# Kernel tuning notes

Measured on AMD Instinct MI355X. Metric: run time of the kernel, lower is better.

The kernel has to match this reference:

```python
import jax, jax.numpy as jnp
import numpy as np

D_MODEL = 1024
NUM_HEADS = 16
HEAD_DIM = D_MODEL // NUM_HEADS


def setup_inputs() -> dict:
    key = jax.random.key(0)
    ks = jax.random.split(key, 9)
    s = 1.0 / np.sqrt(D_MODEL)
    x = jax.random.normal(ks[0], (2, 2048, D_MODEL), dtype=jnp.float32)
    Wq = jax.random.normal(ks[1], (D_MODEL, D_MODEL), dtype=jnp.float32) * s
    Wk = jax.random.normal(ks[2], (D_MODEL, D_MODEL), dtype=jnp.float32) * s
    Wv = jax.random.normal(ks[3], (D_MODEL, D_MODEL), dtype=jnp.float32) * s
    Wo = jax.random.normal(ks[4], (D_MODEL, D_MODEL), dtype=jnp.float32) * s
    bq = jax.random.normal(ks[5], (D_MODEL,), dtype=jnp.float32) * s
    bk = jax.random.normal(ks[6], (D_MODEL,), dtype=jnp.float32) * s
    bv = jax.random.normal(ks[7], (D_MODEL,), dtype=jnp.float32) * s
    bo = jax.random.normal(ks[8], (D_MODEL,), dtype=jnp.float32) * s
    return {"x": x, "Wq": Wq, "bq": bq, "Wk": Wk, "bk": bk, "Wv": Wv, "bv": bv, "Wo": Wo, "bo": bo}


def reference(x, Wq, bq, Wk, bk, Wv, bv, Wo, bo):
    B, S, D = x.shape
    H, Hd = NUM_HEADS, HEAD_DIM
    # QKV projections
    q = (x @ Wq + bq).reshape(B, S, H, Hd).transpose(0, 2, 1, 3)  # [B,H,S,Hd]
    k = (x @ Wk + bk).reshape(B, S, H, Hd).transpose(0, 2, 1, 3)
    v = (x @ Wv + bv).reshape(B, S, H, Hd).transpose(0, 2, 1, 3)
    scores = jnp.einsum("bhqd,bhkd->bhqk", q, k) / jnp.sqrt(jnp.float32(Hd))
    attn = jax.nn.softmax(scores, axis=-1)
    out = jnp.einsum("bhqk,bhkd->bhqd", attn, v)  # [B,H,S,Hd]
    out = out.transpose(0, 2, 1, 3).reshape(B, S, D)
    return out @ Wo + bo
```

## Files before the change

kernel.cpp:

```cpp
#include <hip/hip_runtime.h>
#include <hip/hip_bf16.h>


typedef unsigned short u16;

#define D_MODEL 1024
#define NHEAD 16
#define HDIM 64
#define BATCH 2
#define SEQ 2048
#define MTOT (BATCH * SEQ)

#define QSCALE 0.18033688011112042f

using frag_ab = __attribute__((ext_vector_type(8))) short;
using frag_s4 = __attribute__((ext_vector_type(4))) short;
using frag_cd = __attribute__((ext_vector_type(4))) float;

__device__ __forceinline__ u16 f2u(float f) {
    union { float f; unsigned int i; } x;
    x.f = f;
    unsigned int r = x.i + 0x7fffu + ((x.i >> 16) & 1u);
    return (u16)(r >> 16);
}
__device__ __forceinline__ unsigned int pkrn(float a, float b) {
    union { __hip_bfloat162 h; unsigned int u; } c;
    c.h = __float22bfloat162_rn(float2{a, b});
    return c.u;
}

__global__ void prep(const float* __restrict__ W0, const float* __restrict__ W1,
                     const float* __restrict__ W2, const float* __restrict__ W3,
                     const float* __restrict__ X, u16* __restrict__ Wt,
                     u16* __restrict__ Xb) {
    const int z = blockIdx.z;
    const int tx = threadIdx.x, ty = threadIdx.y;
    if (z < 4) {
        __shared__ u16 t[32][33];
        const float* W = (z == 0) ? W0 : (z == 1) ? W1 : (z == 2) ? W2 : W3;
        u16* o = Wt + (size_t)z * D_MODEL * D_MODEL;
        int n0 = blockIdx.x * 32, k0 = blockIdx.y * 32;
        #pragma unroll
        for (int i = ty; i < 32; i += 8) t[i][tx] = f2u(W[(size_t)(k0 + i) * D_MODEL + n0 + tx]);
        __syncthreads();
        #pragma unroll
        for (int i = ty; i < 32; i += 8) o[(size_t)(n0 + i) * D_MODEL + k0 + tx] = t[tx][i];
    } else {
        int tid = ty * 32 + tx;
        size_t base = ((size_t)(blockIdx.y * 32 + blockIdx.x) * 256 + tid) * 16;
        #pragma unroll
        for (int c = 0; c < 4; ++c) {
            float4 v = *(const float4*)&X[base + c * 4];
            ushort4 o;
            o.x = f2u(v.x); o.y = f2u(v.y); o.z = f2u(v.z); o.w = f2u(v.w);
            *(ushort4*)&Xb[base + c * 4] = o;
        }
    }
}

__launch_bounds__(256, 3)
__global__ void gemm_qkvt(const u16* __restrict__ xb, const u16* __restrict__ Wt,
                          const float* __restrict__ bq, const float* __restrict__ bk,
                          const float* __restrict__ bv, u16* __restrict__ QKw,
                          u16* __restrict__ Vtw) {
    constexpr int BK = 64;
    __shared__ __attribute__((aligned(16))) u16 As[128 * BK];
    __shared__ __attribute__((aligned(16))) u16 Bs[128 * BK];

    const int tid = threadIdx.x;
    const int w = tid >> 6;
    const int lane = tid & 63;
    const int lrow = lane & 15, lquad = lane >> 4;
    const size_t WSZ = (size_t)D_MODEL * D_MODEL;

    const int bid = blockIdx.x;
    const bool vt = bid >= 512;
    const int z = vt ? 2 : (bid >> 8);
    const int t = vt ? (bid - 512) : (bid & 255);
    const int n0 = vt ? (t & 31) * 128 : (t & 7) * 128;
    const int m0 = vt ? (t >> 5) * 128 : (t >> 3) * 128;
    const u16* Ap = vt ? (Wt + 2 * WSZ) : xb;
    const u16* Bp = vt ? xb : (Wt + (size_t)z * WSZ);
    const float* bias = vt ? bv : (z ? bk : bq);

    frag_cd acc[4][4];
    #pragma unroll
    for (int i = 0; i < 4; i++)
        #pragma unroll
        for (int j = 0; j < 4; j++) acc[i][j] = (frag_cd){0.f, 0.f, 0.f, 0.f};

    const int wm = (w >> 1) * 64, wn = (w & 1) * 64;

    for (int k0 = 0; k0 < D_MODEL; k0 += BK) {
        __syncthreads();
        #pragma unroll
        for (int it = 0; it < 4; ++it) {
            int c = it * 256 + tid;
            int r = c >> 3, c8 = c & 7;
            const u16* ga = Ap + (size_t)(m0 + r) * D_MODEL + k0 + c8 * 8;
            char* la = (char*)As + (it * 256 + w * 64) * 16;
            __builtin_amdgcn_global_load_lds((const __attribute__((address_space(1))) void*)ga,
                                             (__attribute__((address_space(3))) void*)la, 16, 0, 0);
            const u16* gb = Bp + (size_t)(n0 + r) * D_MODEL + k0 + c8 * 8;
            char* lb = (char*)Bs + (it * 256 + w * 64) * 16;
            __builtin_amdgcn_global_load_lds((const __attribute__((address_space(1))) void*)gb,
                                             (__attribute__((address_space(3))) void*)lb, 16, 0, 0);
        }
        __syncthreads();

        #pragma unroll
        for (int kc = 0; kc < 2; ++kc) {
            frag_ab av[4], bvv[4];
            #pragma unroll
            for (int i = 0; i < 4; i++)
                av[i] = *(const frag_ab*)&As[(wm + i * 16 + lrow) * BK + kc * 32 + lquad * 8];
            #pragma unroll
            for (int j = 0; j < 4; j++)
                bvv[j] = *(const frag_ab*)&Bs[(wn + j * 16 + lrow) * BK + kc * 32 + lquad * 8];
            #pragma unroll
            for (int i = 0; i < 4; i++)
                #pragma unroll
                for (int j = 0; j < 4; j++)
                    acc[i][j] = __builtin_amdgcn_mfma_f32_16x16x32_bf16(av[i], bvv[j], acc[i][j], 0, 0, 0);
        }
    }

    const float scale = (!vt && z == 0) ? QSCALE : 1.0f;
    #pragma unroll
    for (int j = 0; j < 4; j++) {
        int gn = n0 + wn + j * 16 + lrow;
        #pragma unroll
        for (int i = 0; i < 4; i++) {
            #pragma unroll
            for (int rr = 0; rr < 4; ++rr) {
                int gm = m0 + wm + i * 16 + lquad * 4 + rr;
                if (!vt) {
                    float v = (acc[i][j][rr] + bias[gn]) * scale;
                    u16* oz = QKw + (size_t)z * ((size_t)MTOT * D_MODEL);
                    int b = gm >> 11, s = gm & (SEQ - 1);
                    int h = gn >> 6, d = gn & (HDIM - 1);
                    oz[(((size_t)(b * NHEAD + h)) * SEQ + s) * HDIM + d] = f2u(v);
                } else {
                    float v = acc[i][j][rr] + bias[gm];
                    int h = gm >> 6, d = gm & (HDIM - 1);
                    int b = gn >> 11, s = gn & (SEQ - 1);
                    Vtw[(((size_t)(b * NHEAD + h)) * HDIM + d) * SEQ + s] = f2u(v);
                }
            }
        }
    }
}

__launch_bounds__(256, 2)
__global__ void gemm_out(const u16* __restrict__ A, const u16* __restrict__ Wt,
                         const float* __restrict__ bias, float* __restrict__ out) {
    constexpr int BK = 64;
    __shared__ __attribute__((aligned(16))) u16 As[64 * BK];
    __shared__ __attribute__((aligned(16))) u16 Bs[128 * BK];

    const int tid = threadIdx.x;
    const int w = tid >> 6;
    const int lane = tid & 63;
    const int lrow = lane & 15, lquad = lane >> 4;
    const int m0 = blockIdx.y * 64, n0 = blockIdx.x * 128;

    frag_cd acc[2][4];
    #pragma unroll
    for (int i = 0; i < 2; i++)
        #pragma unroll
        for (int j = 0; j < 4; j++) acc[i][j] = (frag_cd){0.f, 0.f, 0.f, 0.f};

    const int wm = (w >> 1) * 32, wn = (w & 1) * 64;

    for (int k0 = 0; k0 < D_MODEL; k0 += BK) {
        __syncthreads();
        #pragma unroll
        for (int it = 0; it < 2; ++it) {
            int c = it * 256 + tid;
            int r = c >> 3, c8 = c & 7;
            const u16* ga = A + (size_t)(m0 + r) * D_MODEL + k0 + c8 * 8;
            char* la = (char*)As + (it * 256 + w * 64) * 16;
            __builtin_amdgcn_global_load_lds((const __attribute__((address_space(1))) void*)ga,
                                             (__attribute__((address_space(3))) void*)la, 16, 0, 0);
        }
        #pragma unroll
        for (int it = 0; it < 4; ++it) {
            int c = it * 256 + tid;
            int r = c >> 3, c8 = c & 7;
            const u16* gb = Wt + (size_t)(n0 + r) * D_MODEL + k0 + c8 * 8;
            char* lb = (char*)Bs + (it * 256 + w * 64) * 16;
            __builtin_amdgcn_global_load_lds((const __attribute__((address_space(1))) void*)gb,
                                             (__attribute__((address_space(3))) void*)lb, 16, 0, 0);
        }
        __syncthreads();

        #pragma unroll
        for (int kc = 0; kc < 2; ++kc) {
            frag_ab av[2], bvv[4];
            #pragma unroll
            for (int i = 0; i < 2; i++)
                av[i] = *(const frag_ab*)&As[(wm + i * 16 + lrow) * BK + kc * 32 + lquad * 8];
            #pragma unroll
            for (int j = 0; j < 4; j++)
                bvv[j] = *(const frag_ab*)&Bs[(wn + j * 16 + lrow) * BK + kc * 32 + lquad * 8];
            #pragma unroll
            for (int i = 0; i < 2; i++)
                #pragma unroll
                for (int j = 0; j < 4; j++)
                    acc[i][j] = __builtin_amdgcn_mfma_f32_16x16x32_bf16(av[i], bvv[j], acc[i][j], 0, 0, 0);
        }
    }

    #pragma unroll
    for (int j = 0; j < 4; j++) {
        int gn = n0 + wn + j * 16 + lrow;
        float bvf = bias[gn];
        #pragma unroll
        for (int i = 0; i < 2; i++)
            #pragma unroll
            for (int rr = 0; rr < 4; ++rr) {
                int gm = m0 + wm + i * 16 + lquad * 4 + rr;
                out[(size_t)gm * D_MODEL + gn] = acc[i][j][rr] + bvf;
            }
    }
}

__launch_bounds__(512, 4)
__global__ void attn_kernel(const u16* __restrict__ Q, const u16* __restrict__ K,
                            const u16* __restrict__ Vt, u16* __restrict__ O) {
    __shared__ __attribute__((aligned(16))) u16 Ks[2][128 * 64];
    __shared__ __attribute__((aligned(16))) u16 Vs[2][64 * 128];

    const int tid = threadIdx.x;
    const int w = tid >> 6;
    const int lane = tid & 63;
    const int lrow = lane & 15, lquad = lane >> 4;
    const int bh = blockIdx.y;
    const int q0 = blockIdx.x * 128;
    const size_t base = (size_t)bh * SEQ * HDIM;
    const u16* Qg = Q + base;
    const u16* Kg = K + base;
    const u16* Vg = Vt + base;

    frag_ab qf[2];
    #pragma unroll
    for (int kc = 0; kc < 2; ++kc)
        qf[kc] = *(const frag_ab*)&Qg[(size_t)(q0 + w * 16 + lrow) * HDIM + kc * 32 + lquad * 8];

    frag_cd accOT[4];
    #pragma unroll
    for (int df = 0; df < 4; df++) accOT[df] = (frag_cd){0.f, 0.f, 0.f, 0.f};
    float lacc = 0.f;

    auto stage = [&](int bsel, int kt2) {
        const u16* Kt = Kg + (size_t)(kt2 * 128) * HDIM;
        #pragma unroll
        for (int it = 0; it < 2; ++it) {
            const int c = it * 512 + tid;
            const int rk = c >> 3, ck = c & 7;
            const u16* gk = Kt + rk * HDIM + ((ck ^ (rk & 7)) << 3);
            char* lk = (char*)&Ks[bsel][0] + (it * 512 + w * 64) * 16;
            __builtin_amdgcn_global_load_lds((const __attribute__((address_space(1))) void*)gk,
                                             (__attribute__((address_space(3))) void*)lk, 16, 0, 0);
            const int rv = c >> 4, gv = c & 15;
            const u16* gvp = Vg + (size_t)rv * SEQ + kt2 * 128 + ((gv ^ (rv & 7)) << 3);
            char* lv = (char*)&Vs[bsel][0] + (it * 512 + w * 64) * 16;
            __builtin_amdgcn_global_load_lds((const __attribute__((address_space(1))) void*)gvp,
                                             (__attribute__((address_space(3))) void*)lv, 16, 0, 0);
        }
    };

    stage(0, 0);
    __syncthreads();

    int buf = 0;
    for (int kt = 0; kt < SEQ / 128; ++kt) {
        if (kt + 1 < SEQ / 128) stage(buf ^ 1, kt + 1);

        const u16* Ksb = &Ks[buf][0];
        const u16* Vsb = &Vs[buf][0];

        frag_cd sc[8];
        #pragma unroll
        for (int mf = 0; mf < 8; mf++) sc[mf] = (frag_cd){0.f, 0.f, 0.f, 0.f};
        #pragma unroll
        for (int kc = 0; kc < 2; ++kc) {
            const int cswz = (((kc << 2) + lquad) ^ (lrow & 7)) << 3;
            #pragma unroll
            for (int mf = 0; mf < 8; mf++) {
                frag_ab kf = *(const frag_ab*)&Ksb[(mf * 16 + lrow) * 64 + cswz];
                sc[mf] = __builtin_amdgcn_mfma_f32_16x16x32_bf16(kf, qf[kc], sc[mf], 0, 0, 0);
            }
        }

        frag_s4 pk[8];
        #pragma unroll
        for (int mf = 0; mf < 8; mf++) {
            float e0 = exp2f(sc[mf][0]), e1 = exp2f(sc[mf][1]);
            float e2 = exp2f(sc[mf][2]), e3 = exp2f(sc[mf][3]);
            lacc += (e0 + e1) + (e2 + e3);
            union { frag_s4 s; unsigned int u[2]; } pu;
            pu.u[0] = pkrn(e0, e1);
            pu.u[1] = pkrn(e2, e3);
            pk[mf] = pu.s;
        }

        #pragma unroll
        for (int mf = 0; mf < 8; mf++) {
            const int g = 2 * mf + (lquad >> 1);
            #pragma unroll
            for (int df = 0; df < 4; df++) {
                const int dr = df * 16 + lrow;
                frag_s4 vf = *(const frag_s4*)&Vsb[dr * 128 + ((g ^ (lrow & 7)) << 3) + (lquad & 1) * 4];
                accOT[df] = __builtin_amdgcn_mfma_f32_16x16x16bf16_1k(vf, pk[mf], accOT[df], 0, 0, 0);
            }
        }

        __syncthreads();
        buf ^= 1;
    }

    lacc += __shfl_xor(lacc, 16);
    lacc += __shfl_xor(lacc, 32);

    const int b = bh >> 4, h = bh & (NHEAD - 1);
    const int s = q0 + w * 16 + lrow;
    const float inv = 1.0f / lacc;
    u16* orow = O + ((size_t)(b * SEQ + s)) * D_MODEL + h * HDIM;
    #pragma unroll
    for (int df = 0; df < 4; df++) {
        union { unsigned int u[2]; ushort4 s4; } o;
        o.u[0] = pkrn(accOT[df][0] * inv, accOT[df][1] * inv);
        o.u[1] = pkrn(accOT[df][2] * inv, accOT[df][3] * inv);
        *(ushort4*)&orow[df * 16 + lquad * 4] = o.s4;
    }
}

extern "C" void kernel_launch(void* const* d_in, const int* in_sizes, int n_in,
                              void* d_out, int out_size, void* d_ws, size_t ws_size,
                              hipStream_t stream) {
    const float* x  = (const float*)d_in[0];
    const float* Wq = (const float*)d_in[1];
    const float* bq = (const float*)d_in[2];
    const float* Wk = (const float*)d_in[3];
    const float* bk = (const float*)d_in[4];
    const float* Wv = (const float*)d_in[5];
    const float* bv = (const float*)d_in[6];
    const float* Wo = (const float*)d_in[7];
    const float* bo = (const float*)d_in[8];

    u16* ws = (u16*)d_ws;
    const size_t WSZ = (size_t)D_MODEL * D_MODEL;
    const size_t TSZ = (size_t)MTOT * D_MODEL;
    u16* xb  = ws;
    u16* Wt  = ws + 4 * WSZ;
    u16* QKw = ws + 8 * WSZ;
    u16* Vtw = QKw + 2 * TSZ;
    u16* Aw  = Vtw + TSZ;

    prep<<<dim3(32, 32, 5), dim3(32, 8), 0, stream>>>(Wq, Wk, Wv, Wo, x, Wt, xb);
    gemm_qkvt<<<dim3(768), 256, 0, stream>>>(xb, Wt, bq, bk, bv, QKw, Vtw);
    attn_kernel<<<dim3(16, 32), 512, 0, stream>>>(QKw, QKw + TSZ, Vtw, Aw);
    gemm_out<<<dim3(8, 64), 256, 0, stream>>>(Aw, Wt + 3 * WSZ, bo, (float*)d_out);
}
```

Baseline: 218.6 us.

## Give each attention wave two query tiles to reuse K/V fragments

Halves the attention block to 4 waves, with each wave handling two 16-row query groups, so every K and V fragment read from LDS feeds two MFMAs instead of one. The staging loop now runs 4 iterations per thread to fill the same 128-key tile. This is meant to cut LDS read traffic per MFMA and raise arithmetic intensity. In exchange it roughly doubles accumulator and score registers per wave and halves wave-level parallelism per block, which may lower occupancy and latency hiding.

```diff
diff --git a/kernel.cpp b/kernel.cpp
--- a/kernel.cpp
+++ b/kernel.cpp
@@ -225,7 +225,7 @@
     }
 }
 
-__launch_bounds__(512, 4)
+__launch_bounds__(256, 2)
 __global__ void attn_kernel(const u16* __restrict__ Q, const u16* __restrict__ K,
                             const u16* __restrict__ Vt, u16* __restrict__ O) {
     __shared__ __attribute__((aligned(16))) u16 Ks[2][128 * 64];
@@ -242,29 +242,33 @@
     const u16* Kg = K + base;
     const u16* Vg = Vt + base;
 
-    frag_ab qf[2];
-    #pragma unroll
-    for (int kc = 0; kc < 2; ++kc)
-        qf[kc] = *(const frag_ab*)&Qg[(size_t)(q0 + w * 16 + lrow) * HDIM + kc * 32 + lquad * 8];
-
-    frag_cd accOT[4];
-    #pragma unroll
-    for (int df = 0; df < 4; df++) accOT[df] = (frag_cd){0.f, 0.f, 0.f, 0.f};
-    float lacc = 0.f;
+    frag_ab qf[2][2];
+    #pragma unroll
+    for (int g = 0; g < 2; ++g)
+        #pragma unroll
+        for (int kc = 0; kc < 2; ++kc)
+            qf[g][kc] = *(const frag_ab*)&Qg[(size_t)(q0 + g * 64 + w * 16 + lrow) * HDIM + kc * 32 + lquad * 8];
+
+    frag_cd accOT[2][4];
+    #pragma unroll
+    for (int g = 0; g < 2; ++g)
+        #pragma unroll
+        for (int df = 0; df < 4; df++) accOT[g][df] = (frag_cd){0.f, 0.f, 0.f, 0.f};
+    float lacc[2] = {0.f, 0.f};
 
     auto stage = [&](int bsel, int kt2) {
         const u16* Kt = Kg + (size_t)(kt2 * 128) * HDIM;
         #pragma unroll
-        for (int it = 0; it < 2; ++it) {
-            const int c = it * 512 + tid;
+        for (int it = 0; it < 4; ++it) {
+            const int c = it * 256 + tid;
             const int rk = c >> 3, ck = c & 7;
             const u16* gk = Kt + rk * HDIM + ((ck ^ (rk & 7)) << 3);
-            char* lk = (char*)&Ks[bsel][0] + (it * 512 + w * 64) * 16;
+            char* lk = (char*)&Ks[bsel][0] + (it * 256 + w * 64) * 16;
             __builtin_amdgcn_global_load_lds((const __attribute__((address_space(1))) void*)gk,
                                              (__attribute__((address_space(3))) void*)lk, 16, 0, 0);
             const int rv = c >> 4, gv = c & 15;
             const u16* gvp = Vg + (size_t)rv * SEQ + kt2 * 128 + ((gv ^ (rv & 7)) << 3);
-            char* lv = (char*)&Vs[bsel][0] + (it * 512 + w * 64) * 16;
+            char* lv = (char*)&Vs[bsel][0] + (it * 256 + w * 64) * 16;
             __builtin_amdgcn_global_load_lds((const __attribute__((address_space(1))) void*)gvp,
                                              (__attribute__((address_space(3))) void*)lv, 16, 0, 0);
         }
@@ -280,39 +284,45 @@
         const u16* Ksb = &Ks[buf][0];
         const u16* Vsb = &Vs[buf][0];
 
-        frag_cd sc[8];
-        #pragma unroll
-        for (int mf = 0; mf < 8; mf++) sc[mf] = (frag_cd){0.f, 0.f, 0.f, 0.f};
+        frag_cd sc[2][8];
+        #pragma unroll
+        for (int g = 0; g < 2; ++g)
+            #pragma unroll
+            for (int mf = 0; mf < 8; mf++) sc[g][mf] = (frag_cd){0.f, 0.f, 0.f, 0.f};
         #pragma unroll
         for (int kc = 0; kc < 2; ++kc) {
             const int cswz = (((kc << 2) + lquad) ^ (lrow & 7)) << 3;
             #pragma unroll
             for (int mf = 0; mf < 8; mf++) {
                 frag_ab kf = *(const frag_ab*)&Ksb[(mf * 16 + lrow) * 64 + cswz];
-                sc[mf] = __builtin_amdgcn_mfma_f32_16x16x32_bf16(kf, qf[kc], sc[mf], 0, 0, 0);
-            }
-        }
-
-        frag_s4 pk[8];
+                sc[0][mf] = __builtin_amdgcn_mfma_f32_16x16x32_bf16(kf, qf[0][kc], sc[0][mf], 0, 0, 0);
+                sc[1][mf] = __builtin_amdgcn_mfma_f32_16x16x32_bf16(kf, qf[1][kc], sc[1][mf], 0, 0, 0);
+            }
+        }
+
+        frag_s4 pk[2][8];
+        #pragma unroll
+        for (int g = 0; g < 2; ++g)
+            #pragma unroll
+            for (int mf = 0; mf < 8; mf++) {
+                float e0 = exp2f(sc[g][mf][0]), e1 = exp2f(sc[g][mf][1]);
+                float e2 = exp2f(sc[g][mf][2]), e3 = exp2f(sc[g][mf][3]);
+                lacc[g] += (e0 + e1) + (e2 + e3);
+                union { frag_s4 s; unsigned int u[2]; } pu;
+                pu.u[0] = pkrn(e0, e1);
+                pu.u[1] = pkrn(e2, e3);
+                pk[g][mf] = pu.s;
+            }
+
         #pragma unroll
         for (int mf = 0; mf < 8; mf++) {
-            float e0 = exp2f(sc[mf][0]), e1 = exp2f(sc[mf][1]);
-            float e2 = exp2f(sc[mf][2]), e3 = exp2f(sc[mf][3]);
-            lacc += (e0 + e1) + (e2 + e3);
-            union { frag_s4 s; unsigned int u[2]; } pu;
-            pu.u[0] = pkrn(e0, e1);
-            pu.u[1] = pkrn(e2, e3);
-            pk[mf] = pu.s;
-        }
-
-        #pragma unroll
-        for (int mf = 0; mf < 8; mf++) {
-            const int g = 2 * mf + (lquad >> 1);
+            const int gc = 2 * mf + (lquad >> 1);
             #pragma unroll
             for (int df = 0; df < 4; df++) {
                 const int dr = df * 16 + lrow;
-                frag_s4 vf = *(const frag_s4*)&Vsb[dr * 128 + ((g ^ (lrow & 7)) << 3) + (lquad & 1) * 4];
-                accOT[df] = __builtin_amdgcn_mfma_f32_16x16x16bf16_1k(vf, pk[mf], accOT[df], 0, 0, 0);
+                frag_s4 vf = *(const frag_s4*)&Vsb[dr * 128 + ((gc ^ (lrow & 7)) << 3) + (lquad & 1) * 4];
+                accOT[0][df] = __builtin_amdgcn_mfma_f32_16x16x16bf16_1k(vf, pk[0][mf], accOT[0][df], 0, 0, 0);
+                accOT[1][df] = __builtin_amdgcn_mfma_f32_16x16x16bf16_1k(vf, pk[1][mf], accOT[1][df], 0, 0, 0);
             }
         }
 
@@ -320,19 +330,25 @@
         buf ^= 1;
     }
 
-    lacc += __shfl_xor(lacc, 16);
-    lacc += __shfl_xor(lacc, 32);
+    #pragma unroll
+    for (int g = 0; g < 2; ++g) {
+        lacc[g] += __shfl_xor(lacc[g], 16);
+        lacc[g] += __shfl_xor(lacc[g], 32);
+    }
 
     const int b = bh >> 4, h = bh & (NHEAD - 1);
-    const int s = q0 + w * 16 + lrow;
-    const float inv = 1.0f / lacc;
-    u16* orow = O + ((size_t)(b * SEQ + s)) * D_MODEL + h * HDIM;
-    #pragma unroll
-    for (int df = 0; df < 4; df++) {
-        union { unsigned int u[2]; ushort4 s4; } o;
-        o.u[0] = pkrn(accOT[df][0] * inv, accOT[df][1] * inv);
-        o.u[1] = pkrn(accOT[df][2] * inv, accOT[df][3] * inv);
-        *(ushort4*)&orow[df * 16 + lquad * 4] = o.s4;
+    #pragma unroll
+    for (int g = 0; g < 2; ++g) {
+        const int s = q0 + g * 64 + w * 16 + lrow;
+        const float inv = 1.0f / lacc[g];
+        u16* orow = O + ((size_t)(b * SEQ + s)) * D_MODEL + h * HDIM;
+        #pragma unroll
+        for (int df = 0; df < 4; df++) {
+            union { unsigned int u[2]; ushort4 s4; } o;
+            o.u[0] = pkrn(accOT[g][df][0] * inv, accOT[g][df][1] * inv);
+            o.u[1] = pkrn(accOT[g][df][2] * inv, accOT[g][df][3] * inv);
+            *(ushort4*)&orow[df * 16 + lquad * 4] = o.s4;
+        }
     }
 }
 
@@ -360,6 +376,6 @@
 
     prep<<<dim3(32, 32, 5), dim3(32, 8), 0, stream>>>(Wq, Wk, Wv, Wo, x, Wt, xb);
     gemm_qkvt<<<dim3(768), 256, 0, stream>>>(xb, Wt, bq, bk, bv, QKw, Vtw);
-    attn_kernel<<<dim3(16, 32), 512, 0, stream>>>(QKw, QKw + TSZ, Vtw, Aw);
+    attn_kernel<<<dim3(16, 32), 256, 0, stream>>>(QKw, QKw + TSZ, Vtw, Aw);
     gemm_out<<<dim3(8, 64), 256, 0, stream>>>(Aw, Wt + 3 * WSZ, bo, (float*)d_out);
 }
```

Result: slower. 232.4 us (+6.3%).

## Split attention key range across warp halves with single-buffered LDS and combine

Applied to the files above, without the earlier changes.

The attention kernel now gives each block 64 queries instead of 128. Its eight warps form four query groups, and the two halves of the warps each handle half of every 128-key tile. Partial outputs and row sums are combined through LDS at the end. The LDS double buffer is dropped for a single buffer with two barriers per tile, which halves shared memory so that launch bounds can allow 8 blocks. The grid doubles to give more blocks and more occupancy. In exchange, K/V global traffic per query doubles and load latency is no longer overlapped with compute through prefetch.

```diff
diff --git a/kernel.cpp b/kernel.cpp
--- a/kernel.cpp
+++ b/kernel.cpp
@@ -16,6 +16,7 @@
 using frag_ab = __attribute__((ext_vector_type(8))) short;
 using frag_s4 = __attribute__((ext_vector_type(4))) short;
 using frag_cd = __attribute__((ext_vector_type(4))) float;
+using f32x2   = __attribute__((ext_vector_type(2))) float;
 
 __device__ __forceinline__ u16 f2u(float f) {
     union { float f; unsigned int i; } x;
@@ -225,18 +226,21 @@
     }
 }
 
-__launch_bounds__(512, 4)
+__launch_bounds__(512, 8)
 __global__ void attn_kernel(const u16* __restrict__ Q, const u16* __restrict__ K,
                             const u16* __restrict__ Vt, u16* __restrict__ O) {
-    __shared__ __attribute__((aligned(16))) u16 Ks[2][128 * 64];
-    __shared__ __attribute__((aligned(16))) u16 Vs[2][64 * 128];
+    __shared__ __attribute__((aligned(16))) u16 SMEM[16384];
+    u16* Ks = SMEM;
+    u16* Vs = SMEM + 8192;
 
     const int tid = threadIdx.x;
     const int w = tid >> 6;
     const int lane = tid & 63;
     const int lrow = lane & 15, lquad = lane >> 4;
+    const int qg = w & 3;
+    const int kh = w >> 2;
     const int bh = blockIdx.y;
-    const int q0 = blockIdx.x * 128;
+    const int q0 = blockIdx.x * 64;
     const size_t base = (size_t)bh * SEQ * HDIM;
     const u16* Qg = Q + base;
     const u16* Kg = K + base;
@@ -245,94 +249,113 @@
     frag_ab qf[2];
     #pragma unroll
     for (int kc = 0; kc < 2; ++kc)
-        qf[kc] = *(const frag_ab*)&Qg[(size_t)(q0 + w * 16 + lrow) * HDIM + kc * 32 + lquad * 8];
+        qf[kc] = *(const frag_ab*)&Qg[(size_t)(q0 + qg * 16 + lrow) * HDIM + kc * 32 + lquad * 8];
 
     frag_cd accOT[4];
     #pragma unroll
     for (int df = 0; df < 4; df++) accOT[df] = (frag_cd){0.f, 0.f, 0.f, 0.f};
-    float lacc = 0.f;
-
-    auto stage = [&](int bsel, int kt2) {
-        const u16* Kt = Kg + (size_t)(kt2 * 128) * HDIM;
-        #pragma unroll
-        for (int it = 0; it < 2; ++it) {
-            const int c = it * 512 + tid;
-            const int rk = c >> 3, ck = c & 7;
-            const u16* gk = Kt + rk * HDIM + ((ck ^ (rk & 7)) << 3);
-            char* lk = (char*)&Ks[bsel][0] + (it * 512 + w * 64) * 16;
-            __builtin_amdgcn_global_load_lds((const __attribute__((address_space(1))) void*)gk,
-                                             (__attribute__((address_space(3))) void*)lk, 16, 0, 0);
-            const int rv = c >> 4, gv = c & 15;
-            const u16* gvp = Vg + (size_t)rv * SEQ + kt2 * 128 + ((gv ^ (rv & 7)) << 3);
-            char* lv = (char*)&Vs[bsel][0] + (it * 512 + w * 64) * 16;
-            __builtin_amdgcn_global_load_lds((const __attribute__((address_space(1))) void*)gvp,
-                                             (__attribute__((address_space(3))) void*)lv, 16, 0, 0);
-        }
-    };
-
-    stage(0, 0);
-    __syncthreads();
-
-    int buf = 0;
+    f32x2 lacc2 = (f32x2){0.f, 0.f};
+
     for (int kt = 0; kt < SEQ / 128; ++kt) {
-        if (kt + 1 < SEQ / 128) stage(buf ^ 1, kt + 1);
-
-        const u16* Ksb = &Ks[buf][0];
-        const u16* Vsb = &Vs[buf][0];
-
-        frag_cd sc[8];
-        #pragma unroll
-        for (int mf = 0; mf < 8; mf++) sc[mf] = (frag_cd){0.f, 0.f, 0.f, 0.f};
-        #pragma unroll
-        for (int kc = 0; kc < 2; ++kc) {
-            const int cswz = (((kc << 2) + lquad) ^ (lrow & 7)) << 3;
-            #pragma unroll
-            for (int mf = 0; mf < 8; mf++) {
-                frag_ab kf = *(const frag_ab*)&Ksb[(mf * 16 + lrow) * 64 + cswz];
-                sc[mf] = __builtin_amdgcn_mfma_f32_16x16x32_bf16(kf, qf[kc], sc[mf], 0, 0, 0);
-            }
-        }
-
-        frag_s4 pk[8];
-        #pragma unroll
-        for (int mf = 0; mf < 8; mf++) {
-            float e0 = exp2f(sc[mf][0]), e1 = exp2f(sc[mf][1]);
-            float e2 = exp2f(sc[mf][2]), e3 = exp2f(sc[mf][3]);
-            lacc += (e0 + e1) + (e2 + e3);
-            union { frag_s4 s; unsigned int u[2]; } pu;
-            pu.u[0] = pkrn(e0, e1);
-            pu.u[1] = pkrn(e2, e3);
-            pk[mf] = pu.s;
-        }
-
-        #pragma unroll
-        for (int mf = 0; mf < 8; mf++) {
-            const int g = 2 * mf + (lquad >> 1);
-            #pragma unroll
-            for (int df = 0; df < 4; df++) {
-                const int dr = df * 16 + lrow;
-                frag_s4 vf = *(const frag_s4*)&Vsb[dr * 128 + ((g ^ (lrow & 7)) << 3) + (lquad & 1) * 4];
-                accOT[df] = __builtin_amdgcn_mfma_f32_16x16x16bf16_1k(vf, pk[mf], accOT[df], 0, 0, 0);
-            }
-        }
-
-        __syncthreads();
-        buf ^= 1;
-    }
-
+        __syncthreads();
+        {
+            const u16* Kt = Kg + (size_t)(kt * 128) * HDIM;
+            #pragma unroll
+            for (int it = 0; it < 2; ++it) {
+                const int c = it * 512 + tid;
+                const int rk = c >> 3, ck = c & 7;
+                const u16* gk = Kt + rk * HDIM + ((ck ^ (rk & 7)) << 3);
+                char* lk = (char*)Ks + (it * 512 + w * 64) * 16;
+                __builtin_amdgcn_global_load_lds((const __attribute__((address_space(1))) void*)gk,
+                                                 (__attribute__((address_space(3))) void*)lk, 16, 0, 0);
+                const int rv = c >> 4, gv = c & 15;
+                const u16* gvp = Vg + (size_t)rv * SEQ + kt * 128 + ((gv ^ (rv & 7)) << 3);
+                char* lv = (char*)Vs + (it * 512 + w * 64) * 16;
+                __builtin_amdgcn_global_load_lds((const __attribute__((address_space(1))) void*)gvp,
+                                                 (__attribute__((address_space(3))) void*)lv, 16, 0, 0);
+            }
+        }
+        __syncthreads();
+
+        #pragma unroll
+        for (int ch = 0; ch < 2; ++ch) {
+            frag_cd sc[2];
+            #pragma unroll
+            for (int m = 0; m < 2; m++) sc[m] = (frag_cd){0.f, 0.f, 0.f, 0.f};
+            #pragma unroll
+            for (int kc = 0; kc < 2; ++kc) {
+                const int cswz = (((kc << 2) + lquad) ^ (lrow & 7)) << 3;
+                #pragma unroll
+                for (int m = 0; m < 2; m++) {
+                    const int row = kh * 64 + (ch * 2 + m) * 16 + lrow;
+                    frag_ab kf = *(const frag_ab*)&Ks[row * 64 + cswz];
+                    sc[m] = __builtin_amdgcn_mfma_f32_16x16x32_bf16(kf, qf[kc], sc[m], 0, 0, 0);
+                }
+            }
+
+            frag_s4 pk[2];
+            #pragma unroll
+            for (int m = 0; m < 2; m++) {
+                float e0 = exp2f(sc[m][0]), e1 = exp2f(sc[m][1]);
+                float e2 = exp2f(sc[m][2]), e3 = exp2f(sc[m][3]);
+                f32x2 a = {e0, e1}, b2 = {e2, e3};
+                lacc2 += a + b2;
+                union { frag_s4 s; unsigned int u[2]; } pu;
+                pu.u[0] = pkrn(e0, e1);
+                pu.u[1] = pkrn(e2, e3);
+                pk[m] = pu.s;
+            }
+
+            #pragma unroll
+            for (int m = 0; m < 2; m++) {
+                const int gc = ((kh * 4 + ch * 2 + m) << 1) + (lquad >> 1);
+                #pragma unroll
+                for (int df = 0; df < 4; df++) {
+                    const int dr = df * 16 + lrow;
+                    frag_s4 vf = *(const frag_s4*)&Vs[dr * 128 + ((gc ^ (lrow & 7)) << 3) + (lquad & 1) * 4];
+                    accOT[df] = __builtin_amdgcn_mfma_f32_16x16x16bf16_1k(vf, pk[m], accOT[df], 0, 0, 0);
+                }
+            }
+        }
+    }
+
+    float lacc = lacc2[0] + lacc2[1];
     lacc += __shfl_xor(lacc, 16);
     lacc += __shfl_xor(lacc, 32);
 
-    const int b = bh >> 4, h = bh & (NHEAD - 1);
-    const int s = q0 + w * 16 + lrow;
-    const float inv = 1.0f / lacc;
-    u16* orow = O + ((size_t)(b * SEQ + s)) * D_MODEL + h * HDIM;
-    #pragma unroll
-    for (int df = 0; df < 4; df++) {
-        union { unsigned int u[2]; ushort4 s4; } o;
-        o.u[0] = pkrn(accOT[df][0] * inv, accOT[df][1] * inv);
-        o.u[1] = pkrn(accOT[df][2] * inv, accOT[df][3] * inv);
-        *(ushort4*)&orow[df * 16 + lquad * 4] = o.s4;
+    float* comb = (float*)SMEM;
+    float* lsum = (float*)SMEM + 64 * 68;
+    __syncthreads();
+    if (kh) {
+        float* crow = comb + (qg * 16 + lrow) * 68;
+        #pragma unroll
+        for (int df = 0; df < 4; df++)
+            *(float4*)&crow[df * 16 + lquad * 4] =
+                (float4){accOT[df][0], accOT[df][1], accOT[df][2], accOT[df][3]};
+        if (lquad == 0) lsum[qg * 16 + lrow] = lacc;
+    }
+    __syncthreads();
+    if (!kh) {
+        const float* crow = comb + (qg * 16 + lrow) * 68;
+        #pragma unroll
+        for (int df = 0; df < 4; df++) {
+            float4 c = *(const float4*)&crow[df * 16 + lquad * 4];
+            accOT[df][0] += c.x; accOT[df][1] += c.y;
+            accOT[df][2] += c.z; accOT[df][3] += c.w;
+        }
+        lacc += lsum[qg * 16 + lrow];
+
+        const int b = bh >> 4, h = bh & (NHEAD - 1);
+        const int s = q0 + qg * 16 + lrow;
+        const float inv = 1.0f / lacc;
+        u16* orow = O + ((size_t)(b * SEQ + s)) * D_MODEL + h * HDIM;
+        #pragma unroll
+        for (int df = 0; df < 4; df++) {
+            union { unsigned int u[2]; ushort4 s4; } o;
+            o.u[0] = pkrn(accOT[df][0] * inv, accOT[df][1] * inv);
+            o.u[1] = pkrn(accOT[df][2] * inv, accOT[df][3] * inv);
+            *(ushort4*)&orow[df * 16 + lquad * 4] = o.s4;
+        }
     }
 }
 
@@ -360,6 +383,6 @@
 
     prep<<<dim3(32, 32, 5), dim3(32, 8), 0, stream>>>(Wq, Wk, Wv, Wo, x, Wt, xb);
     gemm_qkvt<<<dim3(768), 256, 0, stream>>>(xb, Wt, bq, bk, bv, QKw, Vtw);
-    attn_kernel<<<dim3(16, 32), 512, 0, stream>>>(QKw, QKw + TSZ, Vtw, Aw);
+    attn_kernel<<<dim3(32, 32), 512, 0, stream>>>(QKw, QKw + TSZ, Vtw, Aw);
     gemm_out<<<dim3(8, 64), 256, 0, stream>>>(Aw, Wt + 3 * WSZ, bo, (float*)d_out);
 }
```

New measurement: 223.0 us. 1.02x slower.
